# Optimization experiments

Hardware: AMD Instinct MI355X
Metric: run time of the kernel (lower is better)

Reference implementation:

```python
import jax, jax.numpy as jnp
import numpy as np

EPS = 1e-9
ROUTING_ITERS = 3


def _squash_elem(s):
    # Faithful to source: squash over trailing axis of size 1 => elementwise.
    sq = s * s
    return (sq / (1.0 + sq)) * s / jnp.sqrt(sq + EPS)


def setup_inputs() -> dict:
    key = jax.random.key(0)
    k1, k2 = jax.random.split(key)
    B, I, P = 16, 2048, 16   # batch, num_input_capsules, input_dim_capsules
    O, D = 64, 32            # num_capsules, dim_capsules
    x = jax.random.normal(k1, (B, I, P), dtype=jnp.float32)
    # glorot-ish scale for the transformation weights
    W = jax.random.normal(k2, (1, I, O, D, P), dtype=jnp.float32) * (1.0 / np.sqrt(P))
    bias = jnp.zeros((1, 1, O, D, 1), dtype=jnp.float32)
    return {"x": x, "W": W, "bias": bias}


def reference(x, W, bias):
    # u_hat[b,i,o,d] = sum_p W[0,i,o,d,p] * x[b,i,p]  (the tile+mul+reduce in TF)
    u_hat = jnp.einsum('bip,iodp->biod', x, W[0])
    B, I, O, _ = u_hat.shape
    bias_od = bias[0, 0, :, :, 0]               # [O, D]
    b_logits = jnp.zeros((B, I, O), dtype=u_hat.dtype)
    v = None
    for it in range(ROUTING_ITERS):
        c = jax.nn.softmax(b_logits, axis=2)     # softmax over output capsules
        s = jnp.einsum('bio,biod->bod', c, u_hat) + bias_od
        v = _squash_elem(s)                      # [B, O, D]
        if it < ROUTING_ITERS - 1:
            # agreement[b,i,o] = sum_d u_hat[b,i,o,d] * v[b,o,d]
            b_logits = b_logits + jnp.einsum('biod,bod->bio', u_hat, v)
    return v  # [B, num_capsules, dim_capsules]
```

## Files before the change

### kernel.cpp

```cpp
#include <hip/hip_runtime.h>

#define B_ 16
#define I_ 2048
#define OD_ 2048
#define EPSQ 1e-9f

typedef float v4f __attribute__((ext_vector_type(4)));

__device__ __forceinline__ float squashf(float s) {
  float sq = s * s;
  return sq / (1.0f + sq) * s * rsqrtf(sq + EPSQ);
}

__device__ __forceinline__ float dot4(v4f a, v4f b) {
  return a.x * b.x + a.y * b.y + a.z * b.z + a.w * b.w;
}

__global__ __launch_bounds__(256, 4) void k_uhat(
    const float* __restrict__ x, const float* __restrict__ W,
    float* __restrict__ u, float* __restrict__ part0)
{
  __shared__ float xs[8 * 16 * 16];
  const int t = threadIdx.x;
  const int e = blockIdx.x & 7;
  const int ic = blockIdx.x >> 3;
  const int i0 = ic * 8;
  const int od = e * 256 + t;

  {
    const int b = t >> 4, j = t & 15;
    const float4* src = (const float4*)(x + (size_t)(b * I_ + i0) * 16);
    float4 a0 = src[j * 2], a1 = src[j * 2 + 1];
    const int ii = j >> 1, pq = (j & 1) * 2;
    float4* dst = (float4*)xs + ii * 64 + b * 4;
    dst[pq] = a0; dst[pq + 1] = a1;
  }
  __syncthreads();

  float s0acc[B_];
#pragma unroll
  for (int b = 0; b < B_; ++b) s0acc[b] = 0.f;

  const v4f* wb = (const v4f*)(W + ((size_t)i0 * OD_ + od) * 16);
  v4f wc[4], wn[4];
#pragma unroll
  for (int k = 0; k < 4; ++k) wc[k] = __builtin_nontemporal_load(wb + k);

  for (int ii = 0; ii < 8; ++ii) {
    if (ii < 7) {
      const v4f* wnp = wb + (size_t)(ii + 1) * 8192;
#pragma unroll
      for (int k = 0; k < 4; ++k) wn[k] = __builtin_nontemporal_load(wnp + k);
    }
    const v4f* xv = (const v4f*)xs + ii * 64;
    float* up = u + (size_t)(i0 + ii) * OD_ + od;
#pragma unroll
    for (int b = 0; b < B_; ++b) {
      v4f x0 = xv[b * 4 + 0], x1 = xv[b * 4 + 1];
      v4f x2 = xv[b * 4 + 2], x3 = xv[b * 4 + 3];
      float s = dot4(x0, wc[0]) + dot4(x1, wc[1]) +
                dot4(x2, wc[2]) + dot4(x3, wc[3]);
      up[(size_t)b * I_ * OD_] = s;
      s0acc[b] += s;
    }
    if (ii < 7) {
#pragma unroll
      for (int k = 0; k < 4; ++k) wc[k] = wn[k];
    }
  }
#pragma unroll
  for (int b = 0; b < B_; ++b)
    part0[((size_t)ic * B_ + b) * OD_ + od] = s0acc[b];
}

__global__ __launch_bounds__(256) void k_s0red(
    const float* __restrict__ part0, float* __restrict__ s0)
{
  const int b = blockIdx.x >> 3;
  const int od = (blockIdx.x & 7) * 256 + threadIdx.x;
  float a = 0.f;
  const float* p = part0 + (size_t)b * OD_ + od;
#pragma unroll 8
  for (int ic = 0; ic < 256; ++ic) a += p[(size_t)ic * B_ * OD_];
  s0[b * OD_ + od] = a;
}

__global__ __launch_bounds__(256, 4) void k_route(
    const float* __restrict__ u,
    const float* __restrict__ sA, float scaleA,
    const float* __restrict__ sB,
    const float* __restrict__ bias,
    float* __restrict__ part)
{
  const int t = threadIdx.x;
  const int o = t & 63;
  const int wv = t >> 6;
  const int b = blockIdx.x >> 6;
  const int g = (blockIdx.x & 63) * 4 + wv;
  const int i0 = g * 8;

  v4f vv[8], acc[8];
  {
    const float* sa = sA + b * OD_ + o * 32;
    const float* sb = sB ? sB + b * OD_ + o * 32 : nullptr;
    const float* bp = bias + o * 32;
#pragma unroll
    for (int qq = 0; qq < 8; ++qq) {
#pragma unroll
      for (int j = 0; j < 4; ++j) {
        float bs = bp[qq * 4 + j];
        float val = squashf(sa[qq * 4 + j] * scaleA + bs);
        if (sb) val += squashf(sb[qq * 4 + j] + bs);
        vv[qq][j] = val;
      }
      v4f z = {0.f, 0.f, 0.f, 0.f};
      acc[qq] = z;
    }
  }

  for (int ii = 0; ii < 8; ++ii) {
    const int i = i0 + ii;
    const v4f* up = (const v4f*)(u + (size_t)(b * I_ + i) * OD_ + o * 32);
    v4f r[8];
#pragma unroll
    for (int qq = 0; qq < 8; ++qq) r[qq] = up[qq];

    float logit = 0.f;
#pragma unroll
    for (int qq = 0; qq < 8; ++qq)
#pragma unroll
      for (int j = 0; j < 4; ++j)
        logit = fmaf(r[qq][j], vv[qq][j], logit);

    float m = logit;
#pragma unroll
    for (int off = 32; off > 0; off >>= 1) m = fmaxf(m, __shfl_xor(m, off, 64));
    float ex = __expf(logit - m);
    float sm = ex;
#pragma unroll
    for (int off = 32; off > 0; off >>= 1) sm += __shfl_xor(sm, off, 64);
    float c = ex * __builtin_amdgcn_rcpf(sm);

#pragma unroll
    for (int qq = 0; qq < 8; ++qq)
#pragma unroll
      for (int j = 0; j < 4; ++j)
        acc[qq][j] = fmaf(c, r[qq][j], acc[qq][j]);
  }

  v4f* pp = (v4f*)(part + (size_t)(b * 256 + g) * OD_ + o * 32);
#pragma unroll
  for (int qq = 0; qq < 8; ++qq) pp[qq] = acc[qq];
}

__global__ __launch_bounds__(256) void k_s1red(
    const float* __restrict__ part, float* __restrict__ s1)
{
  const int b = blockIdx.x >> 3;
  const int od = (blockIdx.x & 7) * 256 + threadIdx.x;
  float a = 0.f;
  const float* p = part + (size_t)b * 256 * OD_ + od;
#pragma unroll 8
  for (int g = 0; g < 256; ++g) a += p[(size_t)g * OD_];
  s1[b * OD_ + od] = a;
}

__global__ __launch_bounds__(256) void k_outred(
    const float* __restrict__ part, const float* __restrict__ bias,
    float* __restrict__ out)
{
  const int b = blockIdx.x >> 3;
  const int od = (blockIdx.x & 7) * 256 + threadIdx.x;
  float a = 0.f;
  const float* p = part + (size_t)b * 256 * OD_ + od;
#pragma unroll 8
  for (int g = 0; g < 256; ++g) a += p[(size_t)g * OD_];
  out[b * OD_ + od] = squashf(a + bias[od]);
}

extern "C" void kernel_launch(void* const* d_in, const int* in_sizes, int n_in,
                              void* d_out, int out_size, void* d_ws, size_t ws_size,
                              hipStream_t stream) {
  const float* x = (const float*)d_in[0];
  const float* W = (const float*)d_in[1];
  const float* bias = (const float*)d_in[2];
  float* out = (float*)d_out;

  char* ws = (char*)d_ws;
  float* u_ws  = (float*)ws;
  float* part0 = (float*)(ws + 268435456ull);
  float* part1 = (float*)(ws + 301989888ull);
  float* part2 = part0;
  float* s0    = (float*)(ws + 335544320ull);
  float* s1    = s0 + 32768;

  k_uhat <<<dim3(2048), dim3(256), 0, stream>>>(x, W, u_ws, part0);
  k_s0red<<<dim3(128),  dim3(256), 0, stream>>>(part0, s0);
  k_route<<<dim3(1024), dim3(256), 0, stream>>>(u_ws, s0, 1.0f / 64.0f, nullptr, bias, part1);
  k_s1red<<<dim3(128),  dim3(256), 0, stream>>>(part1, s1);
  k_route<<<dim3(1024), dim3(256), 0, stream>>>(u_ws, s0, 1.0f / 64.0f, s1, bias, part2);
  k_outred<<<dim3(128), dim3(256), 0, stream>>>(part2, bias, out);
}
```

Baseline: 680.9 us.

## Recompute u_hat from W in routing passes instead of materializing it

The change stops writing the 256 MB u_hat tensor. Each routing pass now recomputes u_hat from x and W (128 MB) using W tiles staged into double-buffered LDS via global_load_lds, with each block covering all batches for 8 input capsules. The goal is to cut HBM traffic, since u_hat is written once and read twice. The cost is recomputing the einsum three times, plus 256 large blocks whose LDS use limits occupancy.

Result: faster. 630.0 us (-7.5%).

```diff
diff --git a/kernel.cpp b/kernel.cpp
--- a/kernel.cpp
+++ b/kernel.cpp
@@ -16,9 +16,19 @@
   return a.x * b.x + a.y * b.y + a.z * b.z + a.w * b.w;
 }
 
-__global__ __launch_bounds__(256, 4) void k_uhat(
+__device__ __forceinline__ void gload16(const void* g, void* l) {
+  __builtin_amdgcn_global_load_lds(
+      (__attribute__((address_space(1))) const unsigned int*)g,
+      (__attribute__((address_space(3))) unsigned int*)l, 16, 0, 0);
+}
+
+__device__ __forceinline__ float rfl(float v) {
+  return __uint_as_float(__builtin_amdgcn_readfirstlane(__float_as_uint(v)));
+}
+
+__global__ __launch_bounds__(256, 4) void k_s0sweep(
     const float* __restrict__ x, const float* __restrict__ W,
-    float* __restrict__ u, float* __restrict__ part0)
+    float* __restrict__ part0)
 {
   __shared__ float xs[8 * 16 * 16];
   const int t = threadIdx.x;
@@ -53,15 +63,12 @@
       for (int k = 0; k < 4; ++k) wn[k] = __builtin_nontemporal_load(wnp + k);
     }
     const v4f* xv = (const v4f*)xs + ii * 64;
-    float* up = u + (size_t)(i0 + ii) * OD_ + od;
 #pragma unroll
     for (int b = 0; b < B_; ++b) {
       v4f x0 = xv[b * 4 + 0], x1 = xv[b * 4 + 1];
       v4f x2 = xv[b * 4 + 2], x3 = xv[b * 4 + 3];
-      float s = dot4(x0, wc[0]) + dot4(x1, wc[1]) +
-                dot4(x2, wc[2]) + dot4(x3, wc[3]);
-      up[(size_t)b * I_ * OD_] = s;
-      s0acc[b] += s;
+      s0acc[b] += dot4(x0, wc[0]) + dot4(x1, wc[1]) +
+                  dot4(x2, wc[2]) + dot4(x3, wc[3]);
     }
     if (ii < 7) {
 #pragma unroll
@@ -85,72 +92,155 @@
   s0[b * OD_ + od] = a;
 }
 
-__global__ __launch_bounds__(256, 4) void k_route(
-    const float* __restrict__ u,
+__global__ __launch_bounds__(512, 2) void k_rsweep(
+    const float* __restrict__ x, const float* __restrict__ W,
     const float* __restrict__ sA, float scaleA,
     const float* __restrict__ sB,
     const float* __restrict__ bias,
     float* __restrict__ part)
 {
+  __shared__ float4 bufA[64 * 65];
+  __shared__ float4 bufB[64 * 65];
   const int t = threadIdx.x;
   const int o = t & 63;
   const int wv = t >> 6;
-  const int b = blockIdx.x >> 6;
-  const int g = (blockIdx.x & 63) * 4 + wv;
-  const int i0 = g * 8;
-
-  v4f vv[8], acc[8];
-  {
+  const int i0 = blockIdx.x * 8;
+
+  float vvA[2][16], vvB[2][16];
+#pragma unroll
+  for (int bb = 0; bb < 2; ++bb) {
+    const int b = wv * 2 + bb;
     const float* sa = sA + b * OD_ + o * 32;
     const float* sb = sB ? sB + b * OD_ + o * 32 : nullptr;
     const float* bp = bias + o * 32;
 #pragma unroll
-    for (int qq = 0; qq < 8; ++qq) {
-#pragma unroll
-      for (int j = 0; j < 4; ++j) {
-        float bs = bp[qq * 4 + j];
-        float val = squashf(sa[qq * 4 + j] * scaleA + bs);
-        if (sb) val += squashf(sb[qq * 4 + j] + bs);
-        vv[qq][j] = val;
-      }
-      v4f z = {0.f, 0.f, 0.f, 0.f};
-      acc[qq] = z;
-    }
-  }
+    for (int d = 0; d < 16; ++d) {
+      float bs0 = bp[d], bs1 = bp[d + 16];
+      float va = squashf(sa[d] * scaleA + bs0);
+      float vb = squashf(sa[d + 16] * scaleA + bs1);
+      if (sb) { va += squashf(sb[d] + bs0); vb += squashf(sb[d + 16] + bs1); }
+      vvA[bb][d] = va; vvB[bb][d] = vb;
+    }
+  }
+
+  float accA[2][16], accB[2][16];
+#pragma unroll
+  for (int bb = 0; bb < 2; ++bb)
+#pragma unroll
+    for (int d = 0; d < 16; ++d) { accA[bb][d] = 0.f; accB[bb][d] = 0.f; }
+
+#define STAGE_HALF(row, half, buf)                                         \
+  {                                                                        \
+    const float* rp = (row) + (half) * 256 + o % 64 * 0;   \
+    _Pragma("unroll")                                                      \
+    for (int k = 0; k < 8; ++k) {                                          \
+      const int oo = wv + k * 8;                                           \
+      const float* g = (row) + oo * 512 + (half) * 256 + (t & 63) * 4;     \
+      gload16(g, (void*)((char*)(buf) + (size_t)(oo * 65) * 16));          \
+    }                                                                      \
+    (void)rp;                                                              \
+  }
+
+  const float* Wrow0 = W + (size_t)i0 * (OD_ * 16);
+  STAGE_HALF(Wrow0, 0, bufA);
+  __syncthreads();
+  STAGE_HALF(Wrow0, 1, bufB);
 
   for (int ii = 0; ii < 8; ++ii) {
     const int i = i0 + ii;
-    const v4f* up = (const v4f*)(u + (size_t)(b * I_ + i) * OD_ + o * 32);
-    v4f r[8];
-#pragma unroll
-    for (int qq = 0; qq < 8; ++qq) r[qq] = up[qq];
-
-    float logit = 0.f;
-#pragma unroll
-    for (int qq = 0; qq < 8; ++qq)
-#pragma unroll
-      for (int j = 0; j < 4; ++j)
-        logit = fmaf(r[qq][j], vv[qq][j], logit);
-
-    float m = logit;
-#pragma unroll
-    for (int off = 32; off > 0; off >>= 1) m = fmaxf(m, __shfl_xor(m, off, 64));
-    float ex = __expf(logit - m);
-    float sm = ex;
-#pragma unroll
-    for (int off = 32; off > 0; off >>= 1) sm += __shfl_xor(sm, off, 64);
-    float c = ex * __builtin_amdgcn_rcpf(sm);
-
-#pragma unroll
-    for (int qq = 0; qq < 8; ++qq)
-#pragma unroll
-      for (int j = 0; j < 4; ++j)
-        acc[qq][j] = fmaf(c, r[qq][j], acc[qq][j]);
-  }
-
-  v4f* pp = (v4f*)(part + (size_t)(b * 256 + g) * OD_ + o * 32);
-#pragma unroll
-  for (int qq = 0; qq < 8; ++qq) pp[qq] = acc[qq];
+    const float* Wnext = W + (size_t)(i + 1) * (OD_ * 16);
+
+    float xsv[2][16];
+#pragma unroll
+    for (int bb = 0; bb < 2; ++bb) {
+      const float4* xp = (const float4*)(x + ((size_t)((wv * 2 + bb) * I_) + i) * 16);
+#pragma unroll
+      for (int q = 0; q < 4; ++q) {
+        float4 xq = xp[q];
+        xsv[bb][q * 4 + 0] = rfl(xq.x); xsv[bb][q * 4 + 1] = rfl(xq.y);
+        xsv[bb][q * 4 + 2] = rfl(xq.z); xsv[bb][q * 4 + 3] = rfl(xq.w);
+      }
+    }
+
+    float lg[2] = {0.f, 0.f};
+    float uA[2][16], uB[2][16];
+
+#pragma unroll
+    for (int d = 0; d < 16; ++d) {
+      const float4* wp = bufA + o * 65 + d * 4;
+      float4 w0 = wp[0], w1 = wp[1], w2 = wp[2], w3 = wp[3];
+#pragma unroll
+      for (int bb = 0; bb < 2; ++bb) {
+        float uu = xsv[bb][0] * w0.x;
+        uu = fmaf(xsv[bb][1], w0.y, uu); uu = fmaf(xsv[bb][2], w0.z, uu);
+        uu = fmaf(xsv[bb][3], w0.w, uu); uu = fmaf(xsv[bb][4], w1.x, uu);
+        uu = fmaf(xsv[bb][5], w1.y, uu); uu = fmaf(xsv[bb][6], w1.z, uu);
+        uu = fmaf(xsv[bb][7], w1.w, uu); uu = fmaf(xsv[bb][8], w2.x, uu);
+        uu = fmaf(xsv[bb][9], w2.y, uu); uu = fmaf(xsv[bb][10], w2.z, uu);
+        uu = fmaf(xsv[bb][11], w2.w, uu); uu = fmaf(xsv[bb][12], w3.x, uu);
+        uu = fmaf(xsv[bb][13], w3.y, uu); uu = fmaf(xsv[bb][14], w3.z, uu);
+        uu = fmaf(xsv[bb][15], w3.w, uu);
+        uA[bb][d] = uu;
+        lg[bb] = fmaf(uu, vvA[bb][d], lg[bb]);
+      }
+    }
+    __syncthreads();
+    if (ii < 7) STAGE_HALF(Wnext, 0, bufA);
+
+#pragma unroll
+    for (int d = 0; d < 16; ++d) {
+      const float4* wp = bufB + o * 65 + d * 4;
+      float4 w0 = wp[0], w1 = wp[1], w2 = wp[2], w3 = wp[3];
+#pragma unroll
+      for (int bb = 0; bb < 2; ++bb) {
+        float uu = xsv[bb][0] * w0.x;
+        uu = fmaf(xsv[bb][1], w0.y, uu); uu = fmaf(xsv[bb][2], w0.z, uu);
+        uu = fmaf(xsv[bb][3], w0.w, uu); uu = fmaf(xsv[bb][4], w1.x, uu);
+        uu = fmaf(xsv[bb][5], w1.y, uu); uu = fmaf(xsv[bb][6], w1.z, uu);
+        uu = fmaf(xsv[bb][7], w1.w, uu); uu = fmaf(xsv[bb][8], w2.x, uu);
+        uu = fmaf(xsv[bb][9], w2.y, uu); uu = fmaf(xsv[bb][10], w2.z, uu);
+        uu = fmaf(xsv[bb][11], w2.w, uu); uu = fmaf(xsv[bb][12], w3.x, uu);
+        uu = fmaf(xsv[bb][13], w3.y, uu); uu = fmaf(xsv[bb][14], w3.z, uu);
+        uu = fmaf(xsv[bb][15], w3.w, uu);
+        uB[bb][d] = uu;
+        lg[bb] = fmaf(uu, vvB[bb][d], lg[bb]);
+      }
+    }
+
+#pragma unroll
+    for (int bb = 0; bb < 2; ++bb) {
+      float m = lg[bb];
+#pragma unroll
+      for (int off = 32; off > 0; off >>= 1) m = fmaxf(m, __shfl_xor(m, off, 64));
+      float ex = __expf(lg[bb] - m);
+      float sm = ex;
+#pragma unroll
+      for (int off = 32; off > 0; off >>= 1) sm += __shfl_xor(sm, off, 64);
+      float c = ex * __builtin_amdgcn_rcpf(sm);
+#pragma unroll
+      for (int d = 0; d < 16; ++d) {
+        accA[bb][d] = fmaf(c, uA[bb][d], accA[bb][d]);
+        accB[bb][d] = fmaf(c, uB[bb][d], accB[bb][d]);
+      }
+    }
+    __syncthreads();
+    if (ii < 7) STAGE_HALF(Wnext, 1, bufB);
+  }
+
+#pragma unroll
+  for (int bb = 0; bb < 2; ++bb) {
+    const int b = wv * 2 + bb;
+    float4* dst = (float4*)(part + ((size_t)(b * 256 + blockIdx.x)) * OD_ + o * 32);
+#pragma unroll
+    for (int q = 0; q < 4; ++q) {
+      float4 v0, v1;
+      v0.x = accA[bb][q * 4 + 0]; v0.y = accA[bb][q * 4 + 1];
+      v0.z = accA[bb][q * 4 + 2]; v0.w = accA[bb][q * 4 + 3];
+      v1.x = accB[bb][q * 4 + 0]; v1.y = accB[bb][q * 4 + 1];
+      v1.z = accB[bb][q * 4 + 2]; v1.w = accB[bb][q * 4 + 3];
+      dst[q] = v0; dst[q + 4] = v1;
+    }
+  }
 }
 
 __global__ __launch_bounds__(256) void k_s1red(
@@ -187,17 +277,16 @@
   float* out = (float*)d_out;
 
   char* ws = (char*)d_ws;
-  float* u_ws  = (float*)ws;
-  float* part0 = (float*)(ws + 268435456ull);
-  float* part1 = (float*)(ws + 301989888ull);
+  float* part0 = (float*)ws;
+  float* part1 = (float*)(ws + 33554432ull);
   float* part2 = part0;
-  float* s0    = (float*)(ws + 335544320ull);
+  float* s0    = (float*)(ws + 67108864ull);
   float* s1    = s0 + 32768;
 
-  k_uhat <<<dim3(2048), dim3(256), 0, stream>>>(x, W, u_ws, part0);
-  k_s0red<<<dim3(128),  dim3(256), 0, stream>>>(part0, s0);
-  k_route<<<dim3(1024), dim3(256), 0, stream>>>(u_ws, s0, 1.0f / 64.0f, nullptr, bias, part1);
-  k_s1red<<<dim3(128),  dim3(256), 0, stream>>>(part1, s1);
-  k_route<<<dim3(1024), dim3(256), 0, stream>>>(u_ws, s0, 1.0f / 64.0f, s1, bias, part2);
-  k_outred<<<dim3(128), dim3(256), 0, stream>>>(part2, bias, out);
-}
+  k_s0sweep<<<dim3(2048), dim3(256), 0, stream>>>(x, W, part0);
+  k_s0red  <<<dim3(128),  dim3(256), 0, stream>>>(part0, s0);
+  k_rsweep <<<dim3(256),  dim3(512), 0, stream>>>(x, W, s0, 1.0f / 64.0f, nullptr, bias, part1);
+  k_s1red  <<<dim3(128),  dim3(256), 0, stream>>>(part1, s1);
+  k_rsweep <<<dim3(256),  dim3(512), 0, stream>>>(x, W, s0, 1.0f / 64.0f, s1, bias, part2);
+  k_outred <<<dim3(128),  dim3(256), 0, stream>>>(part2, bias, out);
+}
```
